# Kernel tuning notes

Hardware: AMD Instinct MI355X
Metric: run time of the kernel (lower is better)

The kernel has to match this reference:

```python
import jax, jax.numpy as jnp
import numpy as np

R, B, TAU, SINKHORN_ITERS = 64, 16, 0.5, 5
D_MODEL = 1024
BATCH = 2048


def setup_inputs() -> dict:
    key = jax.random.key(0)
    k1, k2, k3, k4, k5 = jax.random.split(key, 5)
    return {
        "x_t": jax.random.normal(k1, (BATCH, D_MODEL), dtype=jnp.float32),
        "h": jax.random.normal(k2, (BATCH, R * B), dtype=jnp.float32),
        "W_perm": jax.random.normal(k3, (D_MODEL, R * B * B), dtype=jnp.float32) * 0.02,
        "W_diag": jax.random.normal(k4, (D_MODEL, R * B), dtype=jnp.float32) * 0.02,
        "W_alpha": jax.random.normal(k5, (D_MODEL, R * B), dtype=jnp.float32) * 0.02,
    }


def _sinkhorn(log_alpha):
    # 5 iterations of alternating row/col log-normalization
    def body(la, _):
        la = la - jax.nn.logsumexp(la, axis=-1, keepdims=True)
        la = la - jax.nn.logsumexp(la, axis=-2, keepdims=True)
        return la, None
    la, _ = jax.lax.scan(body, log_alpha, None, length=SINKHORN_ITERS)
    return jnp.exp(la)


def reference(x_t, h, W_perm, W_diag, W_alpha):
    batch = x_t.shape[0]
    # (batch, r, b, b) log-space assignment logits
    logits = (x_t @ W_perm).reshape(batch, R, B, B) / TAU
    soft_perm = _sinkhorn(logits)
    # straight-through hard permutation: argmax over rows (dim=-2) per column
    idx = jnp.argmax(soft_perm, axis=-2)                      # (batch, r, b)
    hard = jax.nn.one_hot(idx, B, axis=-2, dtype=soft_perm.dtype)  # (batch, r, b, b)
    perm = jax.lax.stop_gradient(hard - soft_perm) + soft_perm
    h_blocks = h.reshape(batch, R, B)
    h_permuted = jnp.einsum('brij,brj->bri', perm, h_blocks)
    alpha = jax.nn.sigmoid((x_t @ W_alpha)).reshape(batch, R, B)
    diag_vals = alpha * jnp.tanh((x_t @ W_diag).reshape(batch, R, B))
    return (diag_vals * h_permuted).reshape(batch, R * B)
```

## Files before the change

### kernel.cpp

```cpp
#include <hip/hip_runtime.h>


#define D_MODEL 1024
#define RDIM 64
#define BDIM 16
#define NBATCH 2048
#define MB 64
#define XS_LD 68

#define XSZ 2097152
#define WPSZ 16777216
#define WDSZ 2097152

#define OFF_XS   0u
#define OFF_WPS  12582912u
#define OFF_WDS  113246208u
#define OFF_WAS  121634816u
#define WS_NEED  130023424u

typedef __attribute__((ext_vector_type(8))) short short8;
typedef __attribute__((ext_vector_type(4))) float f32x4;
#define MFMA_BF16 __builtin_amdgcn_mfma_f32_16x16x32_bf16

__device__ __forceinline__ unsigned short f2bf_rne(float f) {
    unsigned u = __float_as_uint(f);
    unsigned r = (u + 0x7fffu + ((u >> 16) & 1u)) >> 16;
    return (unsigned short)r;
}
__device__ __forceinline__ float bf2f(unsigned short s) {
    return __uint_as_float(((unsigned)s) << 16);
}

__global__ void k_split_x(const float* __restrict__ x, unsigned short* __restrict__ XS) {
    const int i = blockIdx.x * 256 + threadIdx.x;
    const float v = x[i];
    const unsigned short s1 = f2bf_rne(v);
    const float r1 = v - bf2f(s1);
    const unsigned short s2 = f2bf_rne(r1);
    const float r2 = r1 - bf2f(s2);
    const unsigned short s3 = f2bf_rne(r2);
    XS[i] = s1; XS[XSZ + i] = s2; XS[2 * XSZ + i] = s3;
}

__global__ void k_split_w(const float* __restrict__ W, unsigned short* __restrict__ dst,
                          int C, int colsPerR, int nSplits) {
    __shared__ float tile[32][65];
    const int t = threadIdx.x;
    const int c0 = blockIdx.x * 64;
    const int kt = blockIdx.y;
    #pragma unroll
    for (int i = 0; i < 8; i++) {
        const int k = (t >> 6) * 8 + i;
        tile[k][t & 63] = W[(long)(kt * 32 + k) * C + c0 + (t & 63)];
    }
    __syncthreads();
    const long sliceStride = (long)64 * 32 * colsPerR * 32;
    #pragma unroll
    for (int i = 0; i < 8; i++) {
        const int cl = (t >> 5) * 8 + i;
        const int c = c0 + cl;
        const int rr = c / colsPerR, nn = c % colsPerR;
        const int k = t & 31;
        const float v = tile[k][cl];
        const long off = (((long)(rr * 32 + kt) * colsPerR) + nn) * 32 + k;
        const unsigned short s1 = f2bf_rne(v);
        const float r1 = v - bf2f(s1);
        const unsigned short s2 = f2bf_rne(r1);
        dst[off] = s1;
        dst[sliceStride + off] = s2;
        if (nSplits == 3) {
            const float r2 = r1 - bf2f(s2);
            dst[2 * sliceStride + off] = f2bf_rne(r2);
        }
    }
}

__global__ __launch_bounds__(256, 2)
void bmf_mfma_kernel(const unsigned short* __restrict__ XS,
                     const unsigned short* __restrict__ WPS,
                     const unsigned short* __restrict__ WDS,
                     const unsigned short* __restrict__ WAS,
                     const float* __restrict__ h,
                     float* __restrict__ out)
{
    __shared__ __align__(16) float sm[12800];
    unsigned short* smA = (unsigned short*)sm;
    float* la   = sm;
    float* dval = sm + 8704;
    float* aval = dval + 1024;
    float* hv   = aval + 1024;
    float* hpm  = hv + 1024;

    const int t   = threadIdx.x;
    const int l   = t & 63;
    const int w   = t >> 6;
    const int bid = blockIdx.x;
    const int r   = bid >> 5;
    const int b0  = (bid & 31) * MB;
    const int quad = l >> 4, l15 = l & 15;

    f32x4 acc[4][4];
    f32x4 acc2[2];
    #pragma unroll
    for (int a = 0; a < 4; a++)
        #pragma unroll
        for (int b = 0; b < 4; b++) acc[a][b] = (f32x4){0.f, 0.f, 0.f, 0.f};
    acc2[0] = (f32x4){0.f, 0.f, 0.f, 0.f};
    acc2[1] = (f32x4){0.f, 0.f, 0.f, 0.f};

    const int isAlpha = w >> 1;
    const int mtPair  = w & 1;
    const unsigned short* WX = isAlpha ? WAS : WDS;

    const int srow = t >> 2;
    const int skq  = t & 3;
    int nOff[4];
    #pragma unroll
    for (int ntl = 0; ntl < 4; ntl++) nOff[ntl] = ((w * 4 + ntl) * 16 + l15) * 32 + quad * 8;
    const int w2Off = l15 * 32 + quad * 8;

    short8* sA = (short8*)smA;

    for (int ks = 0; ks < 32; ++ks) {
        const int k0 = ks * 32;
        #pragma unroll
        for (int s = 0; s < 3; s++) {
            const short8 v = *(const short8*)(XS + s * XSZ + (b0 + srow) * D_MODEL + k0 + skq * 8);
            sA[(s * 4 + skq) * 64 + srow] = v;
        }
        __syncthreads();
        short8 bfrag[3][4];
        #pragma unroll
        for (int s = 0; s < 3; s++) {
            const unsigned short* base = WPS + ((long)(s * 64 + r) * 32 + ks) * 8192;
            #pragma unroll
            for (int ntl = 0; ntl < 4; ntl++)
                bfrag[s][ntl] = *(const short8*)(base + nOff[ntl]);
        }
        short8 w2f[2];
        #pragma unroll
        for (int s = 0; s < 2; s++)
            w2f[s] = *(const short8*)(WX + ((long)(s * 64 + r) * 32 + ks) * 512 + w2Off);
        #pragma unroll
        for (int mt = 0; mt < 4; mt++) {
            const short8 a0 = sA[(0 * 4 + quad) * 64 + mt * 16 + l15];
            const short8 a1 = sA[(1 * 4 + quad) * 64 + mt * 16 + l15];
            const short8 a2 = sA[(2 * 4 + quad) * 64 + mt * 16 + l15];
            #pragma unroll
            for (int ntl = 0; ntl < 4; ntl++) {
                f32x4 c = acc[mt][ntl];
                c = MFMA_BF16(a0, bfrag[0][ntl], c, 0, 0, 0);
                c = MFMA_BF16(a0, bfrag[1][ntl], c, 0, 0, 0);
                c = MFMA_BF16(a1, bfrag[0][ntl], c, 0, 0, 0);
                c = MFMA_BF16(a0, bfrag[2][ntl], c, 0, 0, 0);
                c = MFMA_BF16(a1, bfrag[1][ntl], c, 0, 0, 0);
                c = MFMA_BF16(a2, bfrag[0][ntl], c, 0, 0, 0);
                acc[mt][ntl] = c;
            }
            if ((mt >> 1) == mtPair) {
                const int mi = mt & 1;
                f32x4 c2 = acc2[mi];
                c2 = MFMA_BF16(a0, w2f[0], c2, 0, 0, 0);
                c2 = MFMA_BF16(a0, w2f[1], c2, 0, 0, 0);
                c2 = MFMA_BF16(a1, w2f[0], c2, 0, 0, 0);
                acc2[mi] = c2;
            }
        }
        __syncthreads();
    }

    {
        float* arr = isAlpha ? aval : dval;
        #pragma unroll
        for (int mi = 0; mi < 2; mi++) {
            #pragma unroll
            for (int q = 0; q < 4; q++) {
                const int row = (mtPair * 2 + mi) * 16 + quad * 4 + q;
                arr[row * 16 + l15] = acc2[mi][q];
            }
        }
    }
    #pragma unroll
    for (int q = 0; q < 4; q++) {
        const int id  = t + 256 * q;
        const int row = id >> 4, j = id & 15;
        hv[id]  = h[(long)(b0 + row) * D_MODEL + r * BDIM + j];
        hpm[id] = 0.f;
    }
    __syncthreads();

    for (int half = 0; half < 2; ++half) {
        #pragma unroll
        for (int mi = 0; mi < 2; mi++) {
            const int mt = half * 2 + mi;
            #pragma unroll
            for (int ntl = 0; ntl < 4; ntl++) {
                #pragma unroll
                for (int q = 0; q < 4; q++) {
                    const int ml = mi * 16 + quad * 4 + q;
                    la[ml * 272 + (w * 4 + ntl) * 17 + l15] = acc[mt][ntl][q] * 2.0f;
                }
            }
        }
        __syncthreads();

        for (int it = 0; it < 5; ++it) {
            #pragma unroll
            for (int q = 0; q < 2; q++) {
                const int id = t + 256 * q;
                const int m = id >> 4, i = id & 15;
                float* rowp = la + m * 272 + i * 17;
                float mx = rowp[0];
                #pragma unroll
                for (int j = 1; j < 16; j++) mx = fmaxf(mx, rowp[j]);
                float s = 0.f;
                #pragma unroll
                for (int j = 0; j < 16; j++) s += expf(rowp[j] - mx);
                const float lse = mx + logf(s);
                #pragma unroll
                for (int j = 0; j < 16; j++) rowp[j] -= lse;
            }
            __syncthreads();
            #pragma unroll
            for (int q = 0; q < 2; q++) {
                const int id = t + 256 * q;
                const int m = id >> 4, j = id & 15;
                float* colp = la + m * 272 + j;
                float mx = colp[0];
                #pragma unroll
                for (int i = 1; i < 16; i++) mx = fmaxf(mx, colp[i * 17]);
                float s = 0.f;
                #pragma unroll
                for (int i = 0; i < 16; i++) s += expf(colp[i * 17] - mx);
                const float lse = mx + logf(s);
                #pragma unroll
                for (int i = 0; i < 16; i++) colp[i * 17] -= lse;
            }
            __syncthreads();
        }
        #pragma unroll
        for (int q = 0; q < 2; q++) {
            const int id = t + 256 * q;
            const int m = id >> 4, j = id & 15;
            const float* colp = la + m * 272 + j;
            float best = colp[0]; int bi = 0;
            #pragma unroll
            for (int i = 1; i < 16; i++) {
                const float v = colp[i * 17];
                if (v > best) { best = v; bi = i; }
            }
            const int gm = half * 32 + m;
            atomicAdd(&hpm[gm * 16 + bi], hv[gm * 16 + j]);
        }
        __syncthreads();
    }

    #pragma unroll
    for (int q = 0; q < 4; q++) {
        const int id  = t + 256 * q;
        const int row = id >> 4, i = id & 15;
        const float A  = aval[id];
        const float Dv = dval[id];
        const float sg = 1.0f / (1.0f + expf(-A));
        out[(long)(b0 + row) * D_MODEL + r * BDIM + i] = sg * tanhf(Dv) * hpm[id];
    }
}

__global__ __launch_bounds__(256, 2)
void bmf_fused_kernel(const float* __restrict__ x,
                      const float* __restrict__ h,
                      const float* __restrict__ Wp,
                      const float* __restrict__ Wd,
                      const float* __restrict__ Wa,
                      float* __restrict__ out)
{
    __shared__ float sm[15488];
    float* xs   = sm;
    float* wsh  = sm + 32 * XS_LD;
    float* w2s  = wsh + 32 * 256;
    float* la   = sm;
    float* dval = sm + 11392;
    float* aval = dval + 1024;
    float* hv   = aval + 1024;
    float* hpm  = hv + 1024;

    const int t   = threadIdx.x;
    const int bid = blockIdx.x;
    const int r   = bid >> 5;
    const int b0  = (bid & 31) * MB;
    const long rcol0 = (long)r * (BDIM * BDIM);

    const int tr  = t >> 5;
    const int tc  = t & 31;
    const int cAi = tc * 4;
    const int cBi = 128 + tc * 4;
    const int row2 = t >> 2;
    const int c2   = (t & 3) * 8;

    float acc[8][8];
    float acc2[8];
    #pragma unroll
    for (int i = 0; i < 8; i++) {
        acc2[i] = 0.f;
        #pragma unroll
        for (int j = 0; j < 8; j++) acc[i][j] = 0.f;
    }

    for (int ks = 0; ks < D_MODEL / 32; ++ks) {
        const int k0 = ks * 32;
        {
            const int row = t >> 2, kq = t & 3;
            #pragma unroll
            for (int e = 0; e < 2; e++) {
                const int kk = kq * 4 + e * 16;
                const float4 g = *(const float4*)(x + (long)(b0 + row) * D_MODEL + k0 + kk);
                xs[(kk + 0) * XS_LD + row] = g.x;
                xs[(kk + 1) * XS_LD + row] = g.y;
                xs[(kk + 2) * XS_LD + row] = g.z;
                xs[(kk + 3) * XS_LD + row] = g.w;
            }
        }
        {
            const int rbase = t >> 6;
            const int colf  = (t & 63) * 4;
            #pragma unroll
            for (int rep = 0; rep < 8; rep++) {
                const int rowk = rbase + rep * 4;
                const float4 g = *(const float4*)(Wp + (long)(k0 + rowk) * (RDIM * BDIM * BDIM) + rcol0 + colf);
                *(float4*)(wsh + rowk * 256 + colf) = g;
            }
        }
        {
            const int kr = t >> 3;
            const int c  = (t & 7) * 4;
            const float* src = (c < 16)
                ? (Wd + (long)(k0 + kr) * D_MODEL + r * BDIM + c)
                : (Wa + (long)(k0 + kr) * D_MODEL + r * BDIM + (c - 16));
            const float4 g = *(const float4*)src;
            *(float4*)(w2s + kr * 32 + c) = g;
        }
        __syncthreads();
        #pragma unroll
        for (int kk = 0; kk < 32; ++kk) {
            const float4 xlo = *(const float4*)(xs + kk * XS_LD + tr * 8);
            const float4 xhi = *(const float4*)(xs + kk * XS_LD + tr * 8 + 4);
            const float4 wA  = *(const float4*)(wsh + kk * 256 + cAi);
            const float4 wB  = *(const float4*)(wsh + kk * 256 + cBi);
            const float xv[8] = {xlo.x, xlo.y, xlo.z, xlo.w, xhi.x, xhi.y, xhi.z, xhi.w};
            #pragma unroll
            for (int ri = 0; ri < 8; ri++) {
                acc[ri][0] += xv[ri] * wA.x; acc[ri][1] += xv[ri] * wA.y;
                acc[ri][2] += xv[ri] * wA.z; acc[ri][3] += xv[ri] * wA.w;
                acc[ri][4] += xv[ri] * wB.x; acc[ri][5] += xv[ri] * wB.y;
                acc[ri][6] += xv[ri] * wB.z; acc[ri][7] += xv[ri] * wB.w;
            }
            const float xv2 = xs[kk * XS_LD + row2];
            const float4 u0 = *(const float4*)(w2s + kk * 32 + c2);
            const float4 u1 = *(const float4*)(w2s + kk * 32 + c2 + 4);
            acc2[0] += xv2 * u0.x; acc2[1] += xv2 * u0.y;
            acc2[2] += xv2 * u0.z; acc2[3] += xv2 * u0.w;
            acc2[4] += xv2 * u1.x; acc2[5] += xv2 * u1.y;
            acc2[6] += xv2 * u1.z; acc2[7] += xv2 * u1.w;
        }
        __syncthreads();
    }

    #pragma unroll
    for (int e = 0; e < 8; e++) {
        const int c = c2 + e;
        if (c < 16) dval[row2 * 16 + c] = acc2[e];
        else        aval[row2 * 16 + (c - 16)] = acc2[e];
    }
    #pragma unroll
    for (int q = 0; q < 4; q++) {
        const int id  = t + 256 * q;
        const int row = id >> 4, j = id & 15;
        hv[id]  = h[(long)(b0 + row) * D_MODEL + r * BDIM + j];
        hpm[id] = 0.f;
    }
    __syncthreads();

    for (int half = 0; half < 2; ++half) {
        if ((tr >> 2) == half) {
            const int mbase = (tr & 3) * 8;
            #pragma unroll
            for (int ri = 0; ri < 8; ri++) {
                const int m = mbase + ri;
                #pragma unroll
                for (int e = 0; e < 8; e++) {
                    const int col = (e < 4) ? (cAi + e) : (cBi + e - 4);
                    la[m * 272 + (col >> 4) * 17 + (col & 15)] = acc[ri][e] * 2.0f;
                }
            }
        }
        __syncthreads();

        for (int it = 0; it < 5; ++it) {
            #pragma unroll
            for (int q = 0; q < 2; q++) {
                const int id = t + 256 * q;
                const int m = id >> 4, i = id & 15;
                float* rowp = la + m * 272 + i * 17;
                float mx = rowp[0];
                #pragma unroll
                for (int j = 1; j < 16; j++) mx = fmaxf(mx, rowp[j]);
                float s = 0.f;
                #pragma unroll
                for (int j = 0; j < 16; j++) s += expf(rowp[j] - mx);
                const float lse = mx + logf(s);
                #pragma unroll
                for (int j = 0; j < 16; j++) rowp[j] -= lse;
            }
            __syncthreads();
            #pragma unroll
            for (int q = 0; q < 2; q++) {
                const int id = t + 256 * q;
                const int m = id >> 4, j = id & 15;
                float* colp = la + m * 272 + j;
                float mx = colp[0];
                #pragma unroll
                for (int i = 1; i < 16; i++) mx = fmaxf(mx, colp[i * 17]);
                float s = 0.f;
                #pragma unroll
                for (int i = 0; i < 16; i++) s += expf(colp[i * 17] - mx);
                const float lse = mx + logf(s);
                #pragma unroll
                for (int i = 0; i < 16; i++) colp[i * 17] -= lse;
            }
            __syncthreads();
        }
        #pragma unroll
        for (int q = 0; q < 2; q++) {
            const int id = t + 256 * q;
            const int m = id >> 4, j = id & 15;
            const float* colp = la + m * 272 + j;
            float best = colp[0]; int bi = 0;
            #pragma unroll
            for (int i = 1; i < 16; i++) {
                const float v = colp[i * 17];
                if (v > best) { best = v; bi = i; }
            }
            const int gm = half * 32 + m;
            atomicAdd(&hpm[gm * 16 + bi], hv[gm * 16 + j]);
        }
        __syncthreads();
    }

    #pragma unroll
    for (int q = 0; q < 4; q++) {
        const int id  = t + 256 * q;
        const int row = id >> 4, i = id & 15;
        const float A  = aval[id];
        const float Dv = dval[id];
        const float sg = 1.0f / (1.0f + expf(-A));
        out[(long)(b0 + row) * D_MODEL + r * BDIM + i] = sg * tanhf(Dv) * hpm[id];
    }
}

extern "C" void kernel_launch(void* const* d_in, const int* in_sizes, int n_in,
                              void* d_out, int out_size, void* d_ws, size_t ws_size,
                              hipStream_t stream) {
    const float* x  = (const float*)d_in[0];
    const float* h  = (const float*)d_in[1];
    const float* Wp = (const float*)d_in[2];
    const float* Wd = (const float*)d_in[3];
    const float* Wa = (const float*)d_in[4];
    float* out = (float*)d_out;

    if (ws_size >= (size_t)WS_NEED) {
        unsigned short* XS  = (unsigned short*)((char*)d_ws + OFF_XS);
        unsigned short* WPS = (unsigned short*)((char*)d_ws + OFF_WPS);
        unsigned short* WDS = (unsigned short*)((char*)d_ws + OFF_WDS);
        unsigned short* WAS = (unsigned short*)((char*)d_ws + OFF_WAS);
        k_split_x<<<dim3(XSZ / 256), dim3(256), 0, stream>>>(x, XS);
        k_split_w<<<dim3(256, 32), dim3(256), 0, stream>>>(Wp, WPS, 16384, 256, 3);
        k_split_w<<<dim3(16, 32),  dim3(256), 0, stream>>>(Wd, WDS, 1024, 16, 2);
        k_split_w<<<dim3(16, 32),  dim3(256), 0, stream>>>(Wa, WAS, 1024, 16, 2);
        bmf_mfma_kernel<<<dim3(2048), dim3(256), 0, stream>>>(XS, WPS, WDS, WAS, h, out);
    } else {
        bmf_fused_kernel<<<dim3(2048), dim3(256), 0, stream>>>(x, h, Wp, Wd, Wa, out);
    }
}
```

Measured before the change: 595.2 us.

## Load A fragments directly from global, remap block order, use exp2 sinkhorn

The main GEMM loop no longer stages the split x tiles through shared memory. Each wave reads its A fragments straight from global memory, which removes two block barriers per k-step. Block indices are remapped so that eight consecutive blocks share a batch tile across different r, aiming for better L2 reuse of x. Launch bounds go from 2 to 3 waves per SIMD, the Sinkhorn uses exp2/log2 with logits prescaled by 2/ln2, and the two small weight-split launches are merged into one. The risk is redundant global A loads across the four waves and extra register pressure under the tighter occupancy bound.

```diff
diff --git a/kernel.cpp b/kernel.cpp
--- a/kernel.cpp
+++ b/kernel.cpp
@@ -10,13 +10,15 @@
 
 #define XSZ 2097152
 #define WPSZ 16777216
-#define WDSZ 2097152
+#define WDSZ 1048576
 
 #define OFF_XS   0u
 #define OFF_WPS  12582912u
 #define OFF_WDS  113246208u
-#define OFF_WAS  121634816u
-#define WS_NEED  130023424u
+#define OFF_WAS  117440512u
+#define WS_NEED  121634816u
+
+#define LSCALE 2.8853900817779268f
 
 typedef __attribute__((ext_vector_type(8))) short short8;
 typedef __attribute__((ext_vector_type(4))) float f32x4;
@@ -38,12 +40,10 @@
     const float r1 = v - bf2f(s1);
     const unsigned short s2 = f2bf_rne(r1);
     const float r2 = r1 - bf2f(s2);
-    const unsigned short s3 = f2bf_rne(r2);
-    XS[i] = s1; XS[XSZ + i] = s2; XS[2 * XSZ + i] = s3;
-}
-
-__global__ void k_split_w(const float* __restrict__ W, unsigned short* __restrict__ dst,
-                          int C, int colsPerR, int nSplits) {
+    XS[i] = s1; XS[XSZ + i] = s2; XS[2 * XSZ + i] = f2bf_rne(r2);
+}
+
+__global__ void k_split_w(const float* __restrict__ W, unsigned short* __restrict__ dst) {
     __shared__ float tile[32][65];
     const int t = threadIdx.x;
     const int c0 = blockIdx.x * 64;
@@ -51,31 +51,57 @@
     #pragma unroll
     for (int i = 0; i < 8; i++) {
         const int k = (t >> 6) * 8 + i;
-        tile[k][t & 63] = W[(long)(kt * 32 + k) * C + c0 + (t & 63)];
+        tile[k][t & 63] = W[(long)(kt * 32 + k) * 16384 + c0 + (t & 63)];
     }
     __syncthreads();
-    const long sliceStride = (long)64 * 32 * colsPerR * 32;
     #pragma unroll
     for (int i = 0; i < 8; i++) {
         const int cl = (t >> 5) * 8 + i;
         const int c = c0 + cl;
-        const int rr = c / colsPerR, nn = c % colsPerR;
+        const int rr = c >> 8, nn = c & 255;
         const int k = t & 31;
         const float v = tile[k][cl];
-        const long off = (((long)(rr * 32 + kt) * colsPerR) + nn) * 32 + k;
+        const long off = (((long)(rr * 32 + kt) * 256) + nn) * 32 + k;
         const unsigned short s1 = f2bf_rne(v);
         const float r1 = v - bf2f(s1);
         const unsigned short s2 = f2bf_rne(r1);
+        const float r2 = r1 - bf2f(s2);
         dst[off] = s1;
-        dst[sliceStride + off] = s2;
-        if (nSplits == 3) {
-            const float r2 = r1 - bf2f(s2);
-            dst[2 * sliceStride + off] = f2bf_rne(r2);
-        }
-    }
-}
-
-__global__ __launch_bounds__(256, 2)
+        dst[WPSZ + off] = s2;
+        dst[2 * (long)WPSZ + off] = f2bf_rne(r2);
+    }
+}
+
+__global__ void k_split_w2(const float* __restrict__ Wd, const float* __restrict__ Wa,
+                           unsigned short* __restrict__ WDS_, unsigned short* __restrict__ WAS_) {
+    __shared__ float tile[32][65];
+    const float* W = blockIdx.z ? Wa : Wd;
+    unsigned short* dst = blockIdx.z ? WAS_ : WDS_;
+    const int t = threadIdx.x;
+    const int c0 = blockIdx.x * 64;
+    const int kt = blockIdx.y;
+    #pragma unroll
+    for (int i = 0; i < 8; i++) {
+        const int k = (t >> 6) * 8 + i;
+        tile[k][t & 63] = W[(long)(kt * 32 + k) * 1024 + c0 + (t & 63)];
+    }
+    __syncthreads();
+    #pragma unroll
+    for (int i = 0; i < 8; i++) {
+        const int cl = (t >> 5) * 8 + i;
+        const int c = c0 + cl;
+        const int rr = c >> 4, nn = c & 15;
+        const int k = t & 31;
+        const float v = tile[k][cl];
+        const int off = ((rr * 32 + kt) * 16 + nn) * 32 + k;
+        const unsigned short s1 = f2bf_rne(v);
+        const float r1 = v - bf2f(s1);
+        dst[off] = s1;
+        dst[WDSZ + off] = f2bf_rne(r1);
+    }
+}
+
+__global__ __launch_bounds__(256, 3)
 void bmf_mfma_kernel(const unsigned short* __restrict__ XS,
                      const unsigned short* __restrict__ WPS,
                      const unsigned short* __restrict__ WDS,
@@ -84,7 +110,6 @@
                      float* __restrict__ out)
 {
     __shared__ __align__(16) float sm[12800];
-    unsigned short* smA = (unsigned short*)sm;
     float* la   = sm;
     float* dval = sm + 8704;
     float* aval = dval + 1024;
@@ -95,8 +120,9 @@
     const int l   = t & 63;
     const int w   = t >> 6;
     const int bid = blockIdx.x;
-    const int r   = bid >> 5;
-    const int b0  = (bid & 31) * MB;
+    const int r   = ((bid >> 8) << 3) | (bid & 7);
+    const int bt  = (bid >> 3) & 31;
+    const int b0  = bt * MB;
     const int quad = l >> 4, l15 = l & 15;
 
     f32x4 acc[4][4];
@@ -112,61 +138,52 @@
     const int mtPair  = w & 1;
     const unsigned short* WX = isAlpha ? WAS : WDS;
 
-    const int srow = t >> 2;
-    const int skq  = t & 3;
-    int nOff[4];
-    #pragma unroll
-    for (int ntl = 0; ntl < 4; ntl++) nOff[ntl] = ((w * 4 + ntl) * 16 + l15) * 32 + quad * 8;
-    const int w2Off = l15 * 32 + quad * 8;
-
-    short8* sA = (short8*)smA;
+    const unsigned short* aB0 = XS + (b0 + l15) * 1024 + quad * 8;
+    const unsigned short* aB1 = aB0 + XSZ;
+    const unsigned short* aB2 = aB1 + XSZ;
+    const unsigned short* bB0 = WPS + r * 262144 + ((w * 4) * 16 + l15) * 32 + quad * 8;
+    const unsigned short* bB1 = bB0 + WPSZ;
+    const unsigned short* bB2 = bB1 + WPSZ;
+    const unsigned short* wB0 = WX + r * 16384 + l15 * 32 + quad * 8;
+    const unsigned short* wB1 = wB0 + WDSZ;
 
     for (int ks = 0; ks < 32; ++ks) {
-        const int k0 = ks * 32;
-        #pragma unroll
-        for (int s = 0; s < 3; s++) {
-            const short8 v = *(const short8*)(XS + s * XSZ + (b0 + srow) * D_MODEL + k0 + skq * 8);
-            sA[(s * 4 + skq) * 64 + srow] = v;
-        }
-        __syncthreads();
-        short8 bfrag[3][4];
-        #pragma unroll
-        for (int s = 0; s < 3; s++) {
-            const unsigned short* base = WPS + ((long)(s * 64 + r) * 32 + ks) * 8192;
-            #pragma unroll
-            for (int ntl = 0; ntl < 4; ntl++)
-                bfrag[s][ntl] = *(const short8*)(base + nOff[ntl]);
-        }
-        short8 w2f[2];
-        #pragma unroll
-        for (int s = 0; s < 2; s++)
-            w2f[s] = *(const short8*)(WX + ((long)(s * 64 + r) * 32 + ks) * 512 + w2Off);
+        const int bo = ks * 8192;
+        short8 bf0[4], bf1[4], bf2[4];
+        #pragma unroll
+        for (int ntl = 0; ntl < 4; ntl++) {
+            bf0[ntl] = *(const short8*)(bB0 + bo + ntl * 512);
+            bf1[ntl] = *(const short8*)(bB1 + bo + ntl * 512);
+            bf2[ntl] = *(const short8*)(bB2 + bo + ntl * 512);
+        }
+        const short8 wf0 = *(const short8*)(wB0 + ks * 512);
+        const short8 wf1 = *(const short8*)(wB1 + ks * 512);
+        const int ao = ks * 32;
         #pragma unroll
         for (int mt = 0; mt < 4; mt++) {
-            const short8 a0 = sA[(0 * 4 + quad) * 64 + mt * 16 + l15];
-            const short8 a1 = sA[(1 * 4 + quad) * 64 + mt * 16 + l15];
-            const short8 a2 = sA[(2 * 4 + quad) * 64 + mt * 16 + l15];
+            const short8 a0 = *(const short8*)(aB0 + mt * 16384 + ao);
+            const short8 a1 = *(const short8*)(aB1 + mt * 16384 + ao);
+            const short8 a2 = *(const short8*)(aB2 + mt * 16384 + ao);
             #pragma unroll
             for (int ntl = 0; ntl < 4; ntl++) {
                 f32x4 c = acc[mt][ntl];
-                c = MFMA_BF16(a0, bfrag[0][ntl], c, 0, 0, 0);
-                c = MFMA_BF16(a0, bfrag[1][ntl], c, 0, 0, 0);
-                c = MFMA_BF16(a1, bfrag[0][ntl], c, 0, 0, 0);
-                c = MFMA_BF16(a0, bfrag[2][ntl], c, 0, 0, 0);
-                c = MFMA_BF16(a1, bfrag[1][ntl], c, 0, 0, 0);
-                c = MFMA_BF16(a2, bfrag[0][ntl], c, 0, 0, 0);
+                c = MFMA_BF16(a0, bf0[ntl], c, 0, 0, 0);
+                c = MFMA_BF16(a0, bf1[ntl], c, 0, 0, 0);
+                c = MFMA_BF16(a1, bf0[ntl], c, 0, 0, 0);
+                c = MFMA_BF16(a0, bf2[ntl], c, 0, 0, 0);
+                c = MFMA_BF16(a1, bf1[ntl], c, 0, 0, 0);
+                c = MFMA_BF16(a2, bf0[ntl], c, 0, 0, 0);
                 acc[mt][ntl] = c;
             }
             if ((mt >> 1) == mtPair) {
                 const int mi = mt & 1;
                 f32x4 c2 = acc2[mi];
-                c2 = MFMA_BF16(a0, w2f[0], c2, 0, 0, 0);
-                c2 = MFMA_BF16(a0, w2f[1], c2, 0, 0, 0);
-                c2 = MFMA_BF16(a1, w2f[0], c2, 0, 0, 0);
+                c2 = MFMA_BF16(a0, wf0, c2, 0, 0, 0);
+                c2 = MFMA_BF16(a0, wf1, c2, 0, 0, 0);
+                c2 = MFMA_BF16(a1, wf0, c2, 0, 0, 0);
                 acc2[mi] = c2;
             }
         }
-        __syncthreads();
     }
 
     {
@@ -198,7 +215,7 @@
                 #pragma unroll
                 for (int q = 0; q < 4; q++) {
                     const int ml = mi * 16 + quad * 4 + q;
-                    la[ml * 272 + (w * 4 + ntl) * 17 + l15] = acc[mt][ntl][q] * 2.0f;
+                    la[ml * 272 + (w * 4 + ntl) * 17 + l15] = acc[mt][ntl][q] * LSCALE;
                 }
             }
         }
@@ -215,8 +232,8 @@
                 for (int j = 1; j < 16; j++) mx = fmaxf(mx, rowp[j]);
                 float s = 0.f;
                 #pragma unroll
-                for (int j = 0; j < 16; j++) s += expf(rowp[j] - mx);
-                const float lse = mx + logf(s);
+                for (int j = 0; j < 16; j++) s += exp2f(rowp[j] - mx);
+                const float lse = mx + log2f(s);
                 #pragma unroll
                 for (int j = 0; j < 16; j++) rowp[j] -= lse;
             }
@@ -231,8 +248,8 @@
                 for (int i = 1; i < 16; i++) mx = fmaxf(mx, colp[i * 17]);
                 float s = 0.f;
                 #pragma unroll
-                for (int i = 0; i < 16; i++) s += expf(colp[i * 17] - mx);
-                const float lse = mx + logf(s);
+                for (int i = 0; i < 16; i++) s += exp2f(colp[i * 17] - mx);
+                const float lse = mx + log2f(s);
                 #pragma unroll
                 for (int i = 0; i < 16; i++) colp[i * 17] -= lse;
             }
@@ -473,9 +490,8 @@
         unsigned short* WDS = (unsigned short*)((char*)d_ws + OFF_WDS);
         unsigned short* WAS = (unsigned short*)((char*)d_ws + OFF_WAS);
         k_split_x<<<dim3(XSZ / 256), dim3(256), 0, stream>>>(x, XS);
-        k_split_w<<<dim3(256, 32), dim3(256), 0, stream>>>(Wp, WPS, 16384, 256, 3);
-        k_split_w<<<dim3(16, 32),  dim3(256), 0, stream>>>(Wd, WDS, 1024, 16, 2);
-        k_split_w<<<dim3(16, 32),  dim3(256), 0, stream>>>(Wa, WAS, 1024, 16, 2);
+        k_split_w<<<dim3(256, 32), dim3(256), 0, stream>>>(Wp, WPS);
+        k_split_w2<<<dim3(16, 32, 2), dim3(256), 0, stream>>>(Wd, Wa, WDS, WAS);
         bmf_mfma_kernel<<<dim3(2048), dim3(256), 0, stream>>>(XS, WPS, WDS, WAS, h, out);
     } else {
         bmf_fused_kernel<<<dim3(2048), dim3(256), 0, stream>>>(x, h, Wp, Wd, Wa, out);
```

After: 733.8 us. 23.3% more time.
